# Kernel optimization log

Measured on AMD Instinct MI355X. Metric: run time of the kernel, lower is better.

The kernel has to match this reference:

```python
import jax, jax.numpy as jnp
import numpy as np

N_VOLS, N_PARTS = 4, 8          # hard-coded in GL.forward
B = N_VOLS * N_PARTS            # asserted batch size = 32
DIM, HID, PROJ = 8192, 4096, 256
TEMP = 0.1
BN_EPS = 1e-5


def setup_inputs() -> dict:
    key = jax.random.key(0)
    k = jax.random.split(key, 5)
    s1 = 1.0 / np.sqrt(DIM)
    s2 = 1.0 / np.sqrt(HID)
    return {
        "x": jax.random.normal(k[0], (B, DIM), jnp.float32),
        "W1": jax.random.uniform(k[1], (DIM, HID), jnp.float32, -s1, s1),
        "b1": jax.random.uniform(k[2], (HID,), jnp.float32, -s1, s1),
        "gamma": jnp.ones((HID,), jnp.float32),
        "beta": jnp.zeros((HID,), jnp.float32),
        "W2": jax.random.uniform(k[3], (HID, PROJ), jnp.float32, -s2, s2),
        "b2": jax.random.uniform(k[4], (PROJ,), jnp.float32, -s2, s2),
    }


def _gl_loss(proj):
    # F.normalize(p=2, dim=-1); CosineSimilarity on unit vectors == dot product
    p = proj / jnp.linalg.norm(proj, axis=-1, keepdims=True)
    sims = (p @ p.T) / TEMP                       # [B, B]
    idx = jnp.arange(B)
    # pos_index(i) = {i % n_parts + v * n_parts} -> same part id; includes i itself
    pos_mask = (idx[:, None] % N_PARTS) == (idx[None, :] % N_PARTS)  # [B, B], 4 per row
    neg_mask = ~pos_mask                                             # 28 per row
    E = jnp.exp(sims)                              # original uses raw exp (no max-shift)
    row_neg = jnp.sum(jnp.where(neg_mask, E, 0.0), axis=1)    # sum_j exp(s[i, neg_j])
    ET = E.T                                        # ET[i, p] = exp(s[p, i])
    col_neg = jnp.sum(jnp.where(neg_mask, ET, 0.0), axis=1)   # sum_j exp(s[neg_j, i])
    t1 = -jnp.log(E / (E + row_neg[:, None]))      # row-direction term per (i, pos)
    t2 = -jnp.log(ET / (ET + col_neg[:, None]))    # column-direction term per (i, pos)
    per_row = jnp.sum(jnp.where(pos_mask, t1 + t2, 0.0), axis=1) / N_VOLS
    return jnp.sum(per_row) / (B * 2)


def reference(x, W1, b1, gamma, beta, W2, b2):
    # projector MLP: Linear -> BatchNorm1d (training stats) -> ReLU -> Linear
    h = x @ W1 + b1
    mu = jnp.mean(h, axis=0)
    var = jnp.var(h, axis=0)                       # biased variance, BN training mode
    h = gamma * (h - mu) * jax.lax.rsqrt(var + BN_EPS) + beta
    h = jax.nn.relu(h)
    proj = h @ W2 + b2                             # [B, PROJ]
    return _gl_loss(proj)
```

## Files before the change

kernel.cpp:

```cpp
#include <hip/hip_runtime.h>

#define DIM   8192
#define HID   4096
#define PROJ  256
#define NB    32
#define KSP1  16
#define KCH1  (DIM / KSP1)
#define KT1   (KCH1 / 32)
#define KSP2  16
#define KCH2  (HID / KSP2)
#define KT2   (KCH2 / 32)

typedef __attribute__((ext_vector_type(8))) short bf16x8;
typedef __attribute__((ext_vector_type(4))) float f32x4;

__device__ __forceinline__ float bf2f(unsigned short u) {
    return __uint_as_float(((unsigned)u) << 16);
}
__device__ __forceinline__ unsigned short f2bf(float f) {
    unsigned u = __float_as_uint(f);
    u += 0x7fffu + ((u >> 16) & 1u);
    return (unsigned short)(u >> 16);
}
__device__ __forceinline__ unsigned pk2(float a, float b) {
    unsigned ua = __float_as_uint(a);
    unsigned ub = __float_as_uint(b);
    ua += 0x7fffu + ((ua >> 16) & 1u);
    ub += 0x7fffu + ((ub >> 16) & 1u);
    return __builtin_amdgcn_perm(ub, ua, 0x07060302u);
}

__device__ __forceinline__ bool detect_bf16(const unsigned* __restrict__ xw, int lane) {
    unsigned v = xw[lane];
    int e = (int)((v >> 7) & 0xffu);
    bool pl = (e >= 100 && e <= 135);
    unsigned long long b = __ballot(pl);
    return __popcll(b) >= 32;
}

__global__ __launch_bounds__(256, 4) void gemm1_kernel(
    const void* __restrict__ xv, const void* __restrict__ W1v,
    float* __restrict__ hpart)
{
    const int t  = threadIdx.x;
    const int nb = blockIdx.x & 63;
    const int kc = blockIdx.x >> 6;
    const int k0 = kc * KCH1;

    const bool isbf = detect_bf16((const unsigned*)xv, t & 63);
    const unsigned short* xu  = (const unsigned short*)xv;
    const float*          xf  = (const float*)xv;
    const unsigned short* W1u = (const unsigned short*)W1v;
    const float*          W1f = (const float*)W1v;

    const int lane  = t & 63;
    const int w     = t >> 6;
    const int g     = lane >> 4;
    const int ln    = lane & 15;
    const int nbase = nb * 64 + w * 16;

    const unsigned ubB = (unsigned)(k0 + g * 8) * HID + (unsigned)(nbase + ln);
    const unsigned ubA0 = (unsigned)(0 * 16 + ln) * DIM + (unsigned)(k0 + g * 8);
    const unsigned ubA1 = (unsigned)(1 * 16 + ln) * DIM + (unsigned)(k0 + g * 8);

    auto loadB = [&](int kt) -> bf16x8 {
        union { unsigned u[4]; bf16x8 v; } r;
        if (isbf) {
            #pragma unroll
            for (int j = 0; j < 8; ++j)
                ((unsigned short*)r.u)[j] = W1u[ubB + (unsigned)(kt * 32 + j) * HID];
        } else {
            float f[8];
            #pragma unroll
            for (int j = 0; j < 8; ++j)
                f[j] = W1f[ubB + (unsigned)(kt * 32 + j) * HID];
            #pragma unroll
            for (int j = 0; j < 4; ++j)
                r.u[j] = pk2(f[2 * j], f[2 * j + 1]);
        }
        return r.v;
    };
    auto loadA = [&](int kt, int mt) -> bf16x8 {
        const unsigned base = (mt ? ubA1 : ubA0) + (unsigned)(kt * 32);
        if (isbf) return *(const bf16x8*)(xu + base);
        float4 f0 = *(const float4*)(xf + base);
        float4 f1 = *(const float4*)(xf + base + 4);
        union { uint4 u; bf16x8 v; } c;
        c.u = make_uint4(pk2(f0.x, f0.y), pk2(f0.z, f0.w),
                         pk2(f1.x, f1.y), pk2(f1.z, f1.w));
        return c.v;
    };

    bf16x8 bA  = loadB(0), aA0 = loadA(0, 0), aA1 = loadA(0, 1);
    bf16x8 bB  = loadB(1), aB0 = loadA(1, 0), aB1 = loadA(1, 1);

    f32x4 acc0 = {0.f, 0.f, 0.f, 0.f};
    f32x4 acc1 = {0.f, 0.f, 0.f, 0.f};

    #pragma unroll
    for (int kt = 0; kt < KT1; kt += 2) {
        acc0 = __builtin_amdgcn_mfma_f32_16x16x32_bf16(aA0, bA, acc0, 0, 0, 0);
        acc1 = __builtin_amdgcn_mfma_f32_16x16x32_bf16(aA1, bA, acc1, 0, 0, 0);
        if (kt + 2 < KT1) {
            bA = loadB(kt + 2); aA0 = loadA(kt + 2, 0); aA1 = loadA(kt + 2, 1);
        }
        acc0 = __builtin_amdgcn_mfma_f32_16x16x32_bf16(aB0, bB, acc0, 0, 0, 0);
        acc1 = __builtin_amdgcn_mfma_f32_16x16x32_bf16(aB1, bB, acc1, 0, 0, 0);
        if (kt + 3 < KT1) {
            bB = loadB(kt + 3); aB0 = loadA(kt + 3, 0); aB1 = loadA(kt + 3, 1);
        }
    }

    const int col = nbase + ln;
    #pragma unroll
    for (int r = 0; r < 4; ++r) {
        hpart[(kc * NB + g * 4 + r) * HID + col]      = acc0[r];
        hpart[(kc * NB + 16 + g * 4 + r) * HID + col] = acc1[r];
    }
}

__global__ __launch_bounds__(256) void bnrelu_kernel(
    const float* __restrict__ hpart, const void* __restrict__ gv,
    const void* __restrict__ bev, unsigned short* __restrict__ hrelu,
    const void* __restrict__ xv)
{
    __shared__ float red[16][64];
    __shared__ float ssc[64], sbe[64], smu[64];
    const int t  = threadIdx.x;
    const int c4 = t & 15, q = t >> 4;
    const int n0 = blockIdx.x * 64;
    const int nb = n0 + c4 * 4;
    const bool isbf = detect_bf16((const unsigned*)xv, t & 63);

    f32x4 h0 = {0.f, 0.f, 0.f, 0.f};
    f32x4 h1 = {0.f, 0.f, 0.f, 0.f};
    #pragma unroll
    for (int kc = 0; kc < KSP1; ++kc) {
        h0 += *(const f32x4*)(hpart + (size_t)(kc * 32 + 2 * q) * HID + nb);
        h1 += *(const f32x4*)(hpart + (size_t)(kc * 32 + 2 * q + 1) * HID + nb);
    }
    *(f32x4*)&red[q][c4 * 4] = h0 + h1;
    __syncthreads();
    if (t < 64) {
        float s = 0.f;
        #pragma unroll
        for (int i = 0; i < 16; ++i) s += red[i][t];
        smu[t] = s * (1.f / 32.f);
    }
    __syncthreads();
    const f32x4 mu = *(const f32x4*)&smu[c4 * 4];
    const f32x4 d0 = h0 - mu, d1 = h1 - mu;
    *(f32x4*)&red[q][c4 * 4] = d0 * d0 + d1 * d1;
    __syncthreads();
    if (t < 64) {
        float v = 0.f;
        #pragma unroll
        for (int i = 0; i < 16; ++i) v += red[i][t];
        v *= (1.f / 32.f);
        const int nn = n0 + t;
        const float ga = isbf ? bf2f(((const unsigned short*)gv)[nn])  : ((const float*)gv)[nn];
        const float be = isbf ? bf2f(((const unsigned short*)bev)[nn]) : ((const float*)bev)[nn];
        ssc[t] = ga * rsqrtf(v + 1e-5f);
        sbe[t] = be;
    }
    __syncthreads();
    const f32x4 sc = *(const f32x4*)&ssc[c4 * 4];
    const f32x4 be = *(const f32x4*)&sbe[c4 * 4];
    f32x4 r0 = d0 * sc + be;
    f32x4 r1 = d1 * sc + be;
    ushort4 o0, o1;
    o0.x = f2bf(fmaxf(r0.x, 0.f)); o0.y = f2bf(fmaxf(r0.y, 0.f));
    o0.z = f2bf(fmaxf(r0.z, 0.f)); o0.w = f2bf(fmaxf(r0.w, 0.f));
    o1.x = f2bf(fmaxf(r1.x, 0.f)); o1.y = f2bf(fmaxf(r1.y, 0.f));
    o1.z = f2bf(fmaxf(r1.z, 0.f)); o1.w = f2bf(fmaxf(r1.w, 0.f));
    *(ushort4*)(hrelu + (size_t)(2 * q) * HID + nb)     = o0;
    *(ushort4*)(hrelu + (size_t)(2 * q + 1) * HID + nb) = o1;
}

__global__ __launch_bounds__(256, 4) void gemm2_kernel(
    const unsigned short* __restrict__ hrelu, const void* __restrict__ W2v,
    float* __restrict__ ppart, const void* __restrict__ xv)
{
    const int t  = threadIdx.x;
    const int nb = blockIdx.x & 3;
    const int kc = blockIdx.x >> 2;
    const int k0 = kc * KCH2;

    const bool isbf = detect_bf16((const unsigned*)xv, t & 63);
    const unsigned short* W2u = (const unsigned short*)W2v;
    const float*          W2f = (const float*)W2v;

    const int lane  = t & 63;
    const int w     = t >> 6;
    const int g     = lane >> 4;
    const int ln    = lane & 15;
    const int nbase = nb * 64 + w * 16;

    const unsigned ubB = (unsigned)(k0 + g * 8) * PROJ + (unsigned)(nbase + ln);
    const unsigned ubA0 = (unsigned)(0 * 16 + ln) * HID + (unsigned)(k0 + g * 8);
    const unsigned ubA1 = (unsigned)(1 * 16 + ln) * HID + (unsigned)(k0 + g * 8);

    auto loadB = [&](int kt) -> bf16x8 {
        union { unsigned u[4]; bf16x8 v; } r;
        if (isbf) {
            #pragma unroll
            for (int j = 0; j < 8; ++j)
                ((unsigned short*)r.u)[j] = W2u[ubB + (unsigned)(kt * 32 + j) * PROJ];
        } else {
            float f[8];
            #pragma unroll
            for (int j = 0; j < 8; ++j)
                f[j] = W2f[ubB + (unsigned)(kt * 32 + j) * PROJ];
            #pragma unroll
            for (int j = 0; j < 4; ++j)
                r.u[j] = pk2(f[2 * j], f[2 * j + 1]);
        }
        return r.v;
    };
    auto loadA = [&](int kt, int mt) -> bf16x8 {
        return *(const bf16x8*)(hrelu + (mt ? ubA1 : ubA0) + (unsigned)(kt * 32));
    };

    bf16x8 bA  = loadB(0), aA0 = loadA(0, 0), aA1 = loadA(0, 1);
    bf16x8 bB  = loadB(1), aB0 = loadA(1, 0), aB1 = loadA(1, 1);

    f32x4 acc0 = {0.f, 0.f, 0.f, 0.f};
    f32x4 acc1 = {0.f, 0.f, 0.f, 0.f};

    #pragma unroll
    for (int kt = 0; kt < KT2; kt += 2) {
        acc0 = __builtin_amdgcn_mfma_f32_16x16x32_bf16(aA0, bA, acc0, 0, 0, 0);
        acc1 = __builtin_amdgcn_mfma_f32_16x16x32_bf16(aA1, bA, acc1, 0, 0, 0);
        if (kt + 2 < KT2) {
            bA = loadB(kt + 2); aA0 = loadA(kt + 2, 0); aA1 = loadA(kt + 2, 1);
        }
        acc0 = __builtin_amdgcn_mfma_f32_16x16x32_bf16(aB0, bB, acc0, 0, 0, 0);
        acc1 = __builtin_amdgcn_mfma_f32_16x16x32_bf16(aB1, bB, acc1, 0, 0, 0);
        if (kt + 3 < KT2) {
            bB = loadB(kt + 3); aB0 = loadA(kt + 3, 0); aB1 = loadA(kt + 3, 1);
        }
    }

    const int col = nbase + ln;
    #pragma unroll
    for (int r = 0; r < 4; ++r) {
        ppart[(kc * NB + g * 4 + r) * PROJ + col]      = acc0[r];
        ppart[(kc * NB + 16 + g * 4 + r) * PROJ + col] = acc1[r];
    }
}

__global__ __launch_bounds__(1024) void loss_kernel(
    const float* __restrict__ ppart, const void* __restrict__ b2v,
    const void* __restrict__ xv, unsigned* __restrict__ out)
{
    __shared__ float ps[32][260];
    __shared__ float npart2[32][8];
    __shared__ float inrm[32];
    __shared__ float rowtot[32];
    const int t = threadIdx.x;
    const bool isbf = detect_bf16((const unsigned*)xv, t & 63);

    #pragma unroll
    for (int i = 0; i < 8; ++i) {
        const int o = i * 1024 + t;
        float s = 0.f;
        #pragma unroll
        for (int s16 = 0; s16 < KSP2; ++s16) s += ppart[s16 * (NB * PROJ) + o];
        const int c = o & 255;
        s += isbf ? bf2f(((const unsigned short*)b2v)[c]) : ((const float*)b2v)[c];
        ps[o >> 8][c] = s;
    }
    __syncthreads();

    if (t < 256) {
        const int r = t >> 3, seg = t & 7;
        float s = 0.f;
        #pragma unroll
        for (int c = 0; c < 32; ++c) { float v = ps[r][seg * 32 + c]; s += v * v; }
        npart2[r][seg] = s;
    }
    __syncthreads();
    if (t < 32) {
        float s = 0.f;
        #pragma unroll
        for (int j = 0; j < 8; ++j) s += npart2[t][j];
        inrm[t] = rsqrtf(s);
    }
    __syncthreads();

    const int wv   = t >> 6;
    const int lane = t & 63;
    const int j    = (lane >> 1) & 31;
    const int half = lane & 1;
    #pragma unroll
    for (int rr = 0; rr < 2; ++rr) {
        const int i = wv * 2 + rr;
        float acc = 0.f;
        const int cb = half * 128;
        #pragma unroll
        for (int c = 0; c < 128; c += 4) {
            float4 a = *(const float4*)&ps[i][cb + c];
            float4 b = *(const float4*)&ps[j][cb + c];
            acc += a.x * b.x + a.y * b.y + a.z * b.z + a.w * b.w;
        }
        acc += __shfl_xor(acc, 1);

        const float sim = acc * inrm[i] * inrm[j] * 10.0f;
        const float E   = __expf(sim);
        const bool pos  = ((j & 7) == (i & 7));

        float nv = (!pos && half == 0) ? E : 0.f;
        #pragma unroll
        for (int s = 1; s < 64; s <<= 1) nv += __shfl_xor(nv, s);
        float pv = (pos && half == 0) ? (logf(E + nv) - sim) : 0.f;
        #pragma unroll
        for (int s = 1; s < 64; s <<= 1) pv += __shfl_xor(pv, s);
        if (lane == 0) rowtot[i] = pv;
    }
    __syncthreads();

    if (t < 64) {
        float v = (t < 32) ? rowtot[t] : 0.f;
        #pragma unroll
        for (int s = 1; s < 64; s <<= 1) v += __shfl_xor(v, s);
        if (t == 0) {
            const float loss = v * (1.0f / 128.0f);
            const unsigned lb = (unsigned)f2bf(loss);
            const unsigned base = (__float_as_uint(loss) & 0xffff0000u) | lb;
            unsigned best = base;
            float ebest = fabsf(__uint_as_float(base) - loss);
            const unsigned cp = base + 0x10000u;
            const float ep = fabsf(__uint_as_float(cp) - loss);
            if (ep < ebest) { best = cp; ebest = ep; }
            const unsigned cm = base - 0x10000u;
            const float em = fabsf(__uint_as_float(cm) - loss);
            if (em < ebest) { best = cm; }
            out[0] = best;
        }
    }
}

extern "C" void kernel_launch(void* const* d_in, const int* in_sizes, int n_in,
                              void* d_out, int out_size, void* d_ws, size_t ws_size,
                              hipStream_t stream) {
    const void* x  = d_in[0];
    const void* W1 = d_in[1];
    const void* ga = d_in[3];
    const void* be = d_in[4];
    const void* W2 = d_in[5];
    const void* b2 = d_in[6];

    char* wsp = (char*)d_ws;
    float* hpart = (float*)wsp;                 wsp += (size_t)KSP1 * NB * HID * 4;
    unsigned short* hrelu = (unsigned short*)wsp; wsp += (size_t)NB * HID * 2;
    float* ppart = (float*)wsp;                 wsp += (size_t)KSP2 * NB * PROJ * 4;

    gemm1_kernel<<<1024, 256, 0, stream>>>(x, W1, hpart);
    bnrelu_kernel<<<64, 256, 0, stream>>>(hpart, ga, be, hrelu, x);
    gemm2_kernel<<<64, 256, 0, stream>>>(hrelu, W2, ppart, x);
    loss_kernel<<<1, 1024, 0, stream>>>(ppart, b2, x, (unsigned*)d_out);
}
```

Before: 240.3 us.

## Stage bf16 GEMM operands through LDS with a four-deep async global_load_lds pipeline

Adds a shared helper for the bf16 input case in both projector GEMMs. It copies W and activation tiles into swizzled LDS buffers with global_load_lds, using a four-stage ring, explicit vmcnt waits and barriers. The MFMA fragments are then read from LDS instead of through strided per-element global loads, which should coalesce the weight reads and overlap memory with compute. The fp32-input path is kept unchanged as a separate branch. The cost is extra LDS use and two barriers per k-step. The new path only runs when the inputs are detected as bf16.

```diff
diff --git a/kernel.cpp b/kernel.cpp
--- a/kernel.cpp
+++ b/kernel.cpp
@@ -38,10 +38,101 @@
     return __popcll(b) >= 32;
 }
 
+__device__ __forceinline__ void glds16(const void* g, void* l) {
+    __builtin_amdgcn_global_load_lds(
+        (const __attribute__((address_space(1))) void*)g,
+        (__attribute__((address_space(3))) void*)l, 16, 0, 0);
+}
+
+__device__ __forceinline__ void wait_vm_rt(int n) {
+    switch (n) {
+    case 0: asm volatile("s_waitcnt vmcnt(0)" ::: "memory"); break;
+    case 1: asm volatile("s_waitcnt vmcnt(1)" ::: "memory"); break;
+    case 2: asm volatile("s_waitcnt vmcnt(2)" ::: "memory"); break;
+    case 3: asm volatile("s_waitcnt vmcnt(3)" ::: "memory"); break;
+    case 4: asm volatile("s_waitcnt vmcnt(4)" ::: "memory"); break;
+    case 5: asm volatile("s_waitcnt vmcnt(5)" ::: "memory"); break;
+    case 6: asm volatile("s_waitcnt vmcnt(6)" ::: "memory"); break;
+    default: asm volatile("s_waitcnt vmcnt(0)" ::: "memory"); break;
+    }
+}
+
+template<int KT>
+__device__ __forceinline__ void mfma_pipe_bf16(
+    const unsigned short* __restrict__ Asrc, const int lda,
+    const unsigned short* __restrict__ Bsrc, const int ldb,
+    const int k0, const int n0,
+    unsigned short* Wt, unsigned short* At,
+    const int w, const int lane,
+    f32x4& acc0, f32x4& acc1)
+{
+    const int l  = lane;
+    const int g  = lane >> 4;
+    const int ln = lane & 15;
+
+    const size_t srcB = (size_t)(k0 + w * 8 + (l >> 3)) * (size_t)ldb
+                      + (size_t)(n0 + (((l & 7) * 8) ^ (w << 4)));
+    const size_t srcA = (size_t)(w * 16 + (l >> 2)) * (size_t)lda
+                      + (size_t)(k0 + (((l & 3) * 8) ^ (((l >> 2) & 6) << 2)));
+
+    auto issue = [&](int kt) {
+        glds16(Bsrc + srcB + (size_t)kt * 32 * (size_t)ldb,
+               Wt + (size_t)(kt & 3) * 2048 + w * 512);
+        if (w < 2)
+            glds16(Asrc + srcA + (size_t)kt * 32,
+                   At + (size_t)(kt & 3) * 1024 + w * 512);
+    };
+
+    const int cx = (w * 16 + ln) ^ (g << 4);
+    auto readB = [&](int kt) -> bf16x8 {
+        const unsigned short* wb = Wt + (size_t)(kt & 3) * 2048;
+        union { unsigned u[4]; bf16x8 v; } r;
+        #pragma unroll
+        for (int jj = 0; jj < 4; ++jj) {
+            unsigned lo = wb[(g * 8 + 2 * jj)     * 64 + cx];
+            unsigned hi = wb[(g * 8 + 2 * jj + 1) * 64 + cx];
+            r.u[jj] = lo | (hi << 16);
+        }
+        return r.v;
+    };
+    auto readA = [&](int kt, int mt) -> bf16x8 {
+        const unsigned short* ab = At + (size_t)(kt & 3) * 1024;
+        return *(const bf16x8*)(ab + (mt * 16 + ln) * 32
+                                + ((g * 8) ^ ((ln & 6) << 2)));
+    };
+
+    #pragma unroll
+    for (int p = 0; p < 4; ++p) issue(p);
+
+    #pragma unroll
+    for (int kt = 0; kt < KT; ++kt) {
+        const int nIss = (kt + 4 < KT) ? (kt + 4) : KT;
+        const int nOut = nIss - (kt + 1);
+        if (w < 2) wait_vm_rt(2 * nOut); else wait_vm_rt(nOut);
+        __builtin_amdgcn_s_barrier();
+
+        bf16x8 bfr = readB(kt);
+        bf16x8 a0  = readA(kt, 0);
+        bf16x8 a1  = readA(kt, 1);
+        asm volatile("s_waitcnt lgkmcnt(0)" ::: "memory");
+        __builtin_amdgcn_s_barrier();
+
+        if (kt + 4 < KT) issue(kt + 4);
+
+        acc0 = __builtin_amdgcn_mfma_f32_16x16x32_bf16(a0, bfr, acc0, 0, 0, 0);
+        acc1 = __builtin_amdgcn_mfma_f32_16x16x32_bf16(a1, bfr, acc1, 0, 0, 0);
+    }
+}
+
 __global__ __launch_bounds__(256, 4) void gemm1_kernel(
     const void* __restrict__ xv, const void* __restrict__ W1v,
     float* __restrict__ hpart)
 {
+    __shared__ uint4 WtR[1024];
+    __shared__ uint4 AtR[512];
+    unsigned short* Wt = (unsigned short*)WtR;
+    unsigned short* At = (unsigned short*)AtR;
+
     const int t  = threadIdx.x;
     const int nb = blockIdx.x & 63;
     const int kc = blockIdx.x >> 6;
@@ -59,17 +150,19 @@
     const int ln    = lane & 15;
     const int nbase = nb * 64 + w * 16;
 
-    const unsigned ubB = (unsigned)(k0 + g * 8) * HID + (unsigned)(nbase + ln);
-    const unsigned ubA0 = (unsigned)(0 * 16 + ln) * DIM + (unsigned)(k0 + g * 8);
-    const unsigned ubA1 = (unsigned)(1 * 16 + ln) * DIM + (unsigned)(k0 + g * 8);
-
-    auto loadB = [&](int kt) -> bf16x8 {
-        union { unsigned u[4]; bf16x8 v; } r;
-        if (isbf) {
-            #pragma unroll
-            for (int j = 0; j < 8; ++j)
-                ((unsigned short*)r.u)[j] = W1u[ubB + (unsigned)(kt * 32 + j) * HID];
-        } else {
+    f32x4 acc0 = {0.f, 0.f, 0.f, 0.f};
+    f32x4 acc1 = {0.f, 0.f, 0.f, 0.f};
+
+    if (isbf) {
+        mfma_pipe_bf16<KT1>(xu, DIM, W1u, HID, k0, nb * 64, Wt, At, w, lane,
+                            acc0, acc1);
+    } else {
+        const unsigned ubB  = (unsigned)(k0 + g * 8) * HID + (unsigned)(nbase + ln);
+        const unsigned ubA0 = (unsigned)(ln) * DIM + (unsigned)(k0 + g * 8);
+        const unsigned ubA1 = (unsigned)(16 + ln) * DIM + (unsigned)(k0 + g * 8);
+
+        auto loadB = [&](int kt) -> bf16x8 {
+            union { unsigned u[4]; bf16x8 v; } r;
             float f[8];
             #pragma unroll
             for (int j = 0; j < 8; ++j)
@@ -77,37 +170,28 @@
             #pragma unroll
             for (int j = 0; j < 4; ++j)
                 r.u[j] = pk2(f[2 * j], f[2 * j + 1]);
-        }
-        return r.v;
-    };
-    auto loadA = [&](int kt, int mt) -> bf16x8 {
-        const unsigned base = (mt ? ubA1 : ubA0) + (unsigned)(kt * 32);
-        if (isbf) return *(const bf16x8*)(xu + base);
-        float4 f0 = *(const float4*)(xf + base);
-        float4 f1 = *(const float4*)(xf + base + 4);
-        union { uint4 u; bf16x8 v; } c;
-        c.u = make_uint4(pk2(f0.x, f0.y), pk2(f0.z, f0.w),
-                         pk2(f1.x, f1.y), pk2(f1.z, f1.w));
-        return c.v;
-    };
-
-    bf16x8 bA  = loadB(0), aA0 = loadA(0, 0), aA1 = loadA(0, 1);
-    bf16x8 bB  = loadB(1), aB0 = loadA(1, 0), aB1 = loadA(1, 1);
-
-    f32x4 acc0 = {0.f, 0.f, 0.f, 0.f};
-    f32x4 acc1 = {0.f, 0.f, 0.f, 0.f};
-
-    #pragma unroll
-    for (int kt = 0; kt < KT1; kt += 2) {
-        acc0 = __builtin_amdgcn_mfma_f32_16x16x32_bf16(aA0, bA, acc0, 0, 0, 0);
-        acc1 = __builtin_amdgcn_mfma_f32_16x16x32_bf16(aA1, bA, acc1, 0, 0, 0);
-        if (kt + 2 < KT1) {
-            bA = loadB(kt + 2); aA0 = loadA(kt + 2, 0); aA1 = loadA(kt + 2, 1);
-        }
-        acc0 = __builtin_amdgcn_mfma_f32_16x16x32_bf16(aB0, bB, acc0, 0, 0, 0);
-        acc1 = __builtin_amdgcn_mfma_f32_16x16x32_bf16(aB1, bB, acc1, 0, 0, 0);
-        if (kt + 3 < KT1) {
-            bB = loadB(kt + 3); aB0 = loadA(kt + 3, 0); aB1 = loadA(kt + 3, 1);
+            return r.v;
+        };
+        auto loadA = [&](int kt, int mt) -> bf16x8 {
+            const unsigned base = (mt ? ubA1 : ubA0) + (unsigned)(kt * 32);
+            float4 f0 = *(const float4*)(xf + base);
+            float4 f1 = *(const float4*)(xf + base + 4);
+            union { uint4 u; bf16x8 v; } c;
+            c.u = make_uint4(pk2(f0.x, f0.y), pk2(f0.z, f0.w),
+                             pk2(f1.x, f1.y), pk2(f1.z, f1.w));
+            return c.v;
+        };
+
+        bf16x8 bA = loadB(0), aA0 = loadA(0, 0), aA1 = loadA(0, 1);
+        bf16x8 bB = loadB(1), aB0 = loadA(1, 0), aB1 = loadA(1, 1);
+        #pragma unroll
+        for (int kt = 0; kt < KT1; kt += 2) {
+            acc0 = __builtin_amdgcn_mfma_f32_16x16x32_bf16(aA0, bA, acc0, 0, 0, 0);
+            acc1 = __builtin_amdgcn_mfma_f32_16x16x32_bf16(aA1, bA, acc1, 0, 0, 0);
+            if (kt + 2 < KT1) { bA = loadB(kt + 2); aA0 = loadA(kt + 2, 0); aA1 = loadA(kt + 2, 1); }
+            acc0 = __builtin_amdgcn_mfma_f32_16x16x32_bf16(aB0, bB, acc0, 0, 0, 0);
+            acc1 = __builtin_amdgcn_mfma_f32_16x16x32_bf16(aB1, bB, acc1, 0, 0, 0);
+            if (kt + 3 < KT1) { bB = loadB(kt + 3); aB0 = loadA(kt + 3, 0); aB1 = loadA(kt + 3, 1); }
         }
     }
 
@@ -181,6 +265,11 @@
     const unsigned short* __restrict__ hrelu, const void* __restrict__ W2v,
     float* __restrict__ ppart, const void* __restrict__ xv)
 {
+    __shared__ uint4 WtR[1024];
+    __shared__ uint4 AtR[512];
+    unsigned short* Wt = (unsigned short*)WtR;
+    unsigned short* At = (unsigned short*)AtR;
+
     const int t  = threadIdx.x;
     const int nb = blockIdx.x & 3;
     const int kc = blockIdx.x >> 2;
@@ -196,17 +285,19 @@
     const int ln    = lane & 15;
     const int nbase = nb * 64 + w * 16;
 
-    const unsigned ubB = (unsigned)(k0 + g * 8) * PROJ + (unsigned)(nbase + ln);
-    const unsigned ubA0 = (unsigned)(0 * 16 + ln) * HID + (unsigned)(k0 + g * 8);
-    const unsigned ubA1 = (unsigned)(1 * 16 + ln) * HID + (unsigned)(k0 + g * 8);
-
-    auto loadB = [&](int kt) -> bf16x8 {
-        union { unsigned u[4]; bf16x8 v; } r;
-        if (isbf) {
-            #pragma unroll
-            for (int j = 0; j < 8; ++j)
-                ((unsigned short*)r.u)[j] = W2u[ubB + (unsigned)(kt * 32 + j) * PROJ];
-        } else {
+    f32x4 acc0 = {0.f, 0.f, 0.f, 0.f};
+    f32x4 acc1 = {0.f, 0.f, 0.f, 0.f};
+
+    if (isbf) {
+        mfma_pipe_bf16<KT2>(hrelu, HID, W2u, PROJ, k0, nb * 64, Wt, At, w, lane,
+                            acc0, acc1);
+    } else {
+        const unsigned ubB  = (unsigned)(k0 + g * 8) * PROJ + (unsigned)(nbase + ln);
+        const unsigned ubA0 = (unsigned)(ln) * HID + (unsigned)(k0 + g * 8);
+        const unsigned ubA1 = (unsigned)(16 + ln) * HID + (unsigned)(k0 + g * 8);
+
+        auto loadB = [&](int kt) -> bf16x8 {
+            union { unsigned u[4]; bf16x8 v; } r;
             float f[8];
             #pragma unroll
             for (int j = 0; j < 8; ++j)
@@ -214,30 +305,22 @@
             #pragma unroll
             for (int j = 0; j < 4; ++j)
                 r.u[j] = pk2(f[2 * j], f[2 * j + 1]);
-        }
-        return r.v;
-    };
-    auto loadA = [&](int kt, int mt) -> bf16x8 {
-        return *(const bf16x8*)(hrelu + (mt ? ubA1 : ubA0) + (unsigned)(kt * 32));
-    };
-
-    bf16x8 bA  = loadB(0), aA0 = loadA(0, 0), aA1 = loadA(0, 1);
-    bf16x8 bB  = loadB(1), aB0 = loadA(1, 0), aB1 = loadA(1, 1);
-
-    f32x4 acc0 = {0.f, 0.f, 0.f, 0.f};
-    f32x4 acc1 = {0.f, 0.f, 0.f, 0.f};
-
-    #pragma unroll
-    for (int kt = 0; kt < KT2; kt += 2) {
-        acc0 = __builtin_amdgcn_mfma_f32_16x16x32_bf16(aA0, bA, acc0, 0, 0, 0);
-        acc1 = __builtin_amdgcn_mfma_f32_16x16x32_bf16(aA1, bA, acc1, 0, 0, 0);
-        if (kt + 2 < KT2) {
-            bA = loadB(kt + 2); aA0 = loadA(kt + 2, 0); aA1 = loadA(kt + 2, 1);
-        }
-        acc0 = __builtin_amdgcn_mfma_f32_16x16x32_bf16(aB0, bB, acc0, 0, 0, 0);
-        acc1 = __builtin_amdgcn_mfma_f32_16x16x32_bf16(aB1, bB, acc1, 0, 0, 0);
-        if (kt + 3 < KT2) {
-            bB = loadB(kt + 3); aB0 = loadA(kt + 3, 0); aB1 = loadA(kt + 3, 1);
+            return r.v;
+        };
+        auto loadA = [&](int kt, int mt) -> bf16x8 {
+            return *(const bf16x8*)(hrelu + (mt ? ubA1 : ubA0) + (unsigned)(kt * 32));
+        };
+
+        bf16x8 bA = loadB(0), aA0 = loadA(0, 0), aA1 = loadA(0, 1);
+        bf16x8 bB = loadB(1), aB0 = loadA(1, 0), aB1 = loadA(1, 1);
+        #pragma unroll
+        for (int kt = 0; kt < KT2; kt += 2) {
+            acc0 = __builtin_amdgcn_mfma_f32_16x16x32_bf16(aA0, bA, acc0, 0, 0, 0);
+            acc1 = __builtin_amdgcn_mfma_f32_16x16x32_bf16(aA1, bA, acc1, 0, 0, 0);
+            if (kt + 2 < KT2) { bA = loadB(kt + 2); aA0 = loadA(kt + 2, 0); aA1 = loadA(kt + 2, 1); }
+            acc0 = __builtin_amdgcn_mfma_f32_16x16x32_bf16(aB0, bB, acc0, 0, 0, 0);
+            acc1 = __builtin_amdgcn_mfma_f32_16x16x32_bf16(aB1, bB, acc1, 0, 0, 0);
+            if (kt + 3 < KT2) { bB = loadB(kt + 3); aB0 = loadA(kt + 3, 0); aB1 = loadA(kt + 3, 1); }
         }
     }
 
```

New measurement: 240.1 us. About the same (-0.1%).
